# Optimization experiments

Measured on AMD Instinct MI355X. Metric: run time of the kernel, lower is better.

The kernel has to match this reference:

```python
import jax, jax.numpy as jnp
import numpy as np

N_NODES = 50000
N_EDGES = 640000
M_DIM = 128
D_DIM = 128
H_DIM = M_DIM // 2
NORM_EPS = 1e-5


def setup_inputs() -> dict:
    key = jax.random.key(0)
    ks = jax.random.split(key, 8)
    messages = jax.random.normal(ks[0], (N_EDGES, M_DIM), dtype=jnp.float32)
    target_indices = jax.random.randint(ks[1], (N_EDGES,), 0, N_NODES, dtype=jnp.int64)
    node_features = jax.random.normal(ks[2], (N_NODES, D_DIM), dtype=jnp.float32)
    # attention scorer params (torch Linear: weight [out,in])
    W1 = 0.02 * jax.random.normal(ks[3], (H_DIM, M_DIM + D_DIM), dtype=jnp.float32)
    b1 = jnp.zeros((H_DIM,), dtype=jnp.float32)
    W2 = 0.02 * jax.random.normal(ks[4], (1, H_DIM), dtype=jnp.float32)
    gamma = jnp.ones((M_DIM,), dtype=jnp.float32)
    beta = jnp.zeros((M_DIM,), dtype=jnp.float32)
    return {"messages": messages, "target_indices": target_indices,
            "node_features": node_features, "n_nodes": N_NODES,
            "W1": W1, "b1": b1, "W2": W2, "gamma": gamma, "beta": beta}


def reference(messages, target_indices, node_features, n_nodes, W1, b1, W2, gamma, beta):
    # gather target node feats per edge: [E, D]
    target_feats = node_features[target_indices]
    attn_input = jnp.concatenate([messages, target_feats], axis=-1)  # [E, M+D]
    h = jax.nn.gelu(attn_input @ W1.T + b1, approximate=False)       # [E, M//2]
    raw_scores = (h @ W2.T)[:, 0]                                    # [E]
    weights = jax.nn.sigmoid(raw_scores)                             # [E]
    weighted = messages * weights[:, None]                           # [E, M]
    aggregated = jax.ops.segment_sum(weighted, target_indices, num_segments=n_nodes)  # [N, M]
    sum_weights = jax.ops.segment_sum(weights, target_indices, num_segments=n_nodes)  # [N]
    aggregated = aggregated / (sum_weights[:, None] + 1e-8)
    # LayerNorm over last dim
    mu = jnp.mean(aggregated, axis=-1, keepdims=True)
    var = jnp.var(aggregated, axis=-1, keepdims=True)
    normed = (aggregated - mu) * jax.lax.rsqrt(var + NORM_EPS)
    return normed * gamma + beta
```

## Files before the change

kernel.cpp:

```cpp
#include <hip/hip_runtime.h>
#include <hip/hip_bf16.h>

#define EDGES   640000
#define NNODES  50000
#define MDIM    128
#define HDIM    64
#define XSTR    36

typedef __attribute__((ext_vector_type(8))) short bshort8;
typedef __attribute__((ext_vector_type(4))) float f32x4;

__device__ __forceinline__ short f2bf(float f) {
    __hip_bfloat16 h = __float2bfloat16(f);
    return *reinterpret_cast<short*>(&h);
}

__device__ __forceinline__ float gelu_fast(float h) {
    const float x  = h * 0.70710678118654752f;
    const float ax = fabsf(x);
    const float t  = __builtin_amdgcn_rcpf(fmaf(0.3275911f, ax, 1.0f));
    float p = fmaf(1.061405429f, t, -1.453152027f);
    p = fmaf(p, t,  1.421413741f);
    p = fmaf(p, t, -0.284496736f);
    p = fmaf(p, t,  0.254829592f);
    p *= t;
    const float e = __expf(-x * x);
    float er = fmaf(-p, e, 1.0f);
    er = (x < 0.0f) ? -er : er;
    return 0.5f * h * (1.0f + er);
}

__global__ void k0_prep(const float* __restrict__ w1,
                        short* __restrict__ bpack, float* __restrict__ w1dt) {
    const int i = blockIdx.x * 256 + threadIdx.x;
    if (i < 8192) {
        const int ii   = i & 7;
        const int lane = (i >> 3) & 63;
        const int jtkc = i >> 9;
        const int kc = jtkc >> 2, jt = jtkc & 3;
        const int j = jt * 16 + (lane & 15);
        const int k = kc * 32 + (lane >> 4) * 8 + ii;
        bpack[i] = f2bf(w1[j * 256 + k]);
    } else if (i < 16384) {
        const int t = i - 8192;
        const int k = t >> 6, j = t & 63;
        w1dt[t] = w1[j * 256 + 128 + k];
    }
}

__global__ void khist(const int* __restrict__ tgt, int* __restrict__ counts) {
    const int e = blockIdx.x * 256 + threadIdx.x;
    if (e < EDGES) atomicAdd(&counts[tgt[e]], 1);
}

__global__ __launch_bounds__(256, 4) void kg_nodes(
    const float* __restrict__ feats, const float* __restrict__ w1dt,
    const float* __restrict__ b1, float* __restrict__ g)
{
    __shared__ float xs[4][64 * XSTR];
    const int wv = threadIdx.x >> 6, L = threadIdx.x & 63;
    const long base = ((long)blockIdx.x * 4 + wv) * 64;
    float* xb = xs[wv];
    float h[HDIM];
#pragma unroll
    for (int j = 0; j < HDIM; ++j) h[j] = 0.0f;
    const int gq = L >> 3, sub = L & 7;
    for (int c = 0; c < 4; ++c) {
        const int col0 = c * 32;
#pragma unroll
        for (int r = 0; r < 8; ++r) {
            long row = base + gq + 8 * r;
            if (row > NNODES - 1) row = NNODES - 1;
            float4 v = *(const float4*)(feats + row * MDIM + col0 + sub * 4);
            *(float4*)(xb + (gq + 8 * r) * XSTR + sub * 4) = v;
        }
        __syncthreads();
        for (int k4 = 0; k4 < 8; ++k4) {
            const float4 xv = *(const float4*)(xb + L * XSTR + 4 * k4);
            const float* colw = w1dt + (c * 32 + 4 * k4) * HDIM;
            const float xa[4] = {xv.x, xv.y, xv.z, xv.w};
#pragma unroll
            for (int kk = 0; kk < 4; ++kk) {
                const float xk = xa[kk];
#pragma unroll
                for (int j = 0; j < HDIM; ++j)
                    h[j] = fmaf(colw[kk * HDIM + j], xk, h[j]);
            }
        }
        __syncthreads();
    }
    const long row = base + L;
    if (row < NNODES) {
        float* gp = g + row * HDIM;
#pragma unroll
        for (int j4 = 0; j4 < 16; ++j4) {
            float4 b4 = *(const float4*)(b1 + 4 * j4);
            float4 o;
            o.x = h[4 * j4 + 0] + b4.x; o.y = h[4 * j4 + 1] + b4.y;
            o.z = h[4 * j4 + 2] + b4.z; o.w = h[4 * j4 + 3] + b4.w;
            *(float4*)(gp + 4 * j4) = o;
        }
    }
}

__global__ void kscan_local(const int* __restrict__ counts, int* __restrict__ offsets,
                            int* __restrict__ blocksums) {
    __shared__ int s[256];
    const int tid = threadIdx.x;
    const int i = blockIdx.x * 256 + tid;
    int v = (i < NNODES) ? counts[i] : 0;
    s[tid] = v;
    __syncthreads();
    for (int d = 1; d < 256; d <<= 1) {
        int t = (tid >= d) ? s[tid - d] : 0;
        __syncthreads();
        s[tid] += t;
        __syncthreads();
    }
    if (i < NNODES) offsets[i] = s[tid];
    if (tid == 255) blocksums[blockIdx.x] = s[255];
}

__global__ void kscan_blk(int* __restrict__ blocksums, int nblk) {
    __shared__ int s[256];
    const int tid = threadIdx.x;
    int v = (tid < nblk) ? blocksums[tid] : 0;
    s[tid] = v;
    __syncthreads();
    for (int d = 1; d < 256; d <<= 1) {
        int t = (tid >= d) ? s[tid - d] : 0;
        __syncthreads();
        s[tid] += t;
        __syncthreads();
    }
    if (tid < nblk) blocksums[tid] = s[tid] - v;
}

__global__ void kscan_fix(int* __restrict__ offsets, const int* __restrict__ blocksums,
                          const int* __restrict__ counts, int* __restrict__ cursor) {
    const int i = blockIdx.x * 256 + threadIdx.x;
    if (i < NNODES) {
        const int incl = offsets[i] + blocksums[i >> 8];
        offsets[i] = incl;
        cursor[i] = incl - counts[i];
    }
}

__global__ void kscatter(const int* __restrict__ tgt, int* __restrict__ cursor,
                         int* __restrict__ eidx) {
    const int e = blockIdx.x * 256 + threadIdx.x;
    if (e < EDGES) {
        const int pos = atomicAdd(&cursor[tgt[e]], 1);
        eidx[pos] = e;
    }
}

__global__ __launch_bounds__(256, 4) void kfused(
    const float* __restrict__ msgs, const int* __restrict__ eidx,
    const int* __restrict__ offsets, const short* __restrict__ bpack,
    const float* __restrict__ g, const float* __restrict__ w2,
    const float* __restrict__ gamma, const float* __restrict__ beta,
    float* __restrict__ out)
{
    __shared__ float lds[4][16][132];
    const int wv = threadIdx.x >> 6, L = threadIdx.x & 63;
    const int node = blockIdx.x * 4 + wv;
    if (node >= NNODES) return;
    const int end = offsets[node];
    const int beg = (node == 0) ? 0 : offsets[node - 1];
    const int m = end - beg;

    const int n = L & 15, quad = L >> 4;
    float (*xb)[132] = lds[wv];
    const bshort8* bp = (const bshort8*)bpack;

    float w2v[4], gv[4];
    const float* gp = g + (long)node * HDIM;
#pragma unroll
    for (int jt = 0; jt < 4; ++jt) {
        w2v[jt] = w2[jt * 16 + n];
        gv[jt]  = gp[jt * 16 + n];
    }

    float2 acc = {0.0f, 0.0f};
    float swl = 0.0f;

    for (int t0 = 0; t0 < m; t0 += 16) {
        const int sn = t0 + n;
        const int eid = eidx[beg + ((sn < m) ? sn : 0)];
        const float* rp = msgs + (long)eid * MDIM;

        float4 v[8];
#pragma unroll
        for (int kc = 0; kc < 4; ++kc) {
            v[2 * kc]     = *(const float4*)(rp + kc * 32 + quad * 8);
            v[2 * kc + 1] = *(const float4*)(rp + kc * 32 + quad * 8 + 4);
        }
#pragma unroll
        for (int kc = 0; kc < 4; ++kc) {
            *(float4*)(&xb[n][kc * 32 + quad * 8])     = v[2 * kc];
            *(float4*)(&xb[n][kc * 32 + quad * 8 + 4]) = v[2 * kc + 1];
        }

        f32x4 hacc[4];
#pragma unroll
        for (int jt = 0; jt < 4; ++jt) hacc[jt] = (f32x4){0.f, 0.f, 0.f, 0.f};
#pragma unroll
        for (int kc = 0; kc < 4; ++kc) {
            const float4 va = v[2 * kc], vb = v[2 * kc + 1];
            bshort8 a;
            a[0] = f2bf(va.x); a[1] = f2bf(va.y); a[2] = f2bf(va.z); a[3] = f2bf(va.w);
            a[4] = f2bf(vb.x); a[5] = f2bf(vb.y); a[6] = f2bf(vb.z); a[7] = f2bf(vb.w);
#pragma unroll
            for (int jt = 0; jt < 4; ++jt)
                hacc[jt] = __builtin_amdgcn_mfma_f32_16x16x32_bf16(a, bp[(kc * 4 + jt) * 64 + L], hacc[jt], 0, 0, 0);
        }

        float wq[4];
#pragma unroll
        for (int r = 0; r < 4; ++r) {
            float raw = 0.0f;
#pragma unroll
            for (int jt = 0; jt < 4; ++jt) {
                const float hj = hacc[jt][r] + gv[jt];
                raw = fmaf(gelu_fast(hj), w2v[jt], raw);
            }
#pragma unroll
            for (int off = 1; off < 16; off <<= 1)
                raw += __shfl_xor(raw, off, 64);
            const int slot = t0 + quad * 4 + r;
            wq[r] = (slot < m) ? __builtin_amdgcn_rcpf(1.0f + __expf(-raw)) : 0.0f;
        }

#pragma unroll
        for (int i = 0; i < 16; ++i) {
            const float wi = __shfl(wq[i & 3], (i >> 2) << 4, 64);
            swl += wi;
            const float2 mv = *(const float2*)(&xb[i][2 * L]);
            acc.x = fmaf(mv.x, wi, acc.x);
            acc.y = fmaf(mv.y, wi, acc.y);
        }
    }

    float s1 = acc.x + acc.y;
    float s2 = acc.x * acc.x + acc.y * acc.y;
#pragma unroll
    for (int off = 32; off; off >>= 1) {
        s1 += __shfl_xor(s1, off, 64);
        s2 += __shfl_xor(s2, off, 64);
    }
    const float inv = 1.0f / (swl + 1e-8f);
    float2 a;
    a.x = acc.x * inv; a.y = acc.y * inv;
    const float mu = s1 * inv * (1.0f / MDIM);
    const float var = s2 * inv * inv * (1.0f / MDIM) - mu * mu;
    const float rs = rsqrtf(var + 1e-5f);
    const float2 gm = *(const float2*)(gamma + 2 * L);
    const float2 bt = *(const float2*)(beta + 2 * L);
    float2 o;
    o.x = (a.x - mu) * rs * gm.x + bt.x;
    o.y = (a.y - mu) * rs * gm.y + bt.y;
    *(float2*)(out + (long)node * MDIM + 2 * L) = o;
}

extern "C" void kernel_launch(void* const* d_in, const int* in_sizes, int n_in,
                              void* d_out, int out_size, void* d_ws, size_t ws_size,
                              hipStream_t stream) {
    const float* msgs  = (const float*)d_in[0];
    const int*   tgt   = (const int*)d_in[1];
    const float* feats = (const float*)d_in[2];
    const float* W1    = (const float*)d_in[4];
    const float* b1    = (const float*)d_in[5];
    const float* W2    = (const float*)d_in[6];
    const float* gamma = (const float*)d_in[7];
    const float* beta  = (const float*)d_in[8];
    float* out = (float*)d_out;

    char* ws = (char*)d_ws;
    short* bpack   = (short*)(ws + 0);
    float* w1dt    = (float*)(ws + (32 << 10));
    int*   counts  = (int*)  (ws + (64 << 10));
    int*   offsets = (int*)  (ws + (320 << 10));
    int*   cursor  = (int*)  (ws + (576 << 10));
    int*   bsums   = (int*)  (ws + (832 << 10));
    int*   eidx    = (int*)  (ws + (4 << 20));
    float* g       = (float*)(ws + (8 << 20));

    hipMemsetAsync(counts, 0, NNODES * sizeof(int), stream);

    k0_prep<<<64, 256, 0, stream>>>(W1, bpack, w1dt);
    khist<<<(EDGES + 255) / 256, 256, 0, stream>>>(tgt, counts);
    kg_nodes<<<(NNODES + 255) / 256, 256, 0, stream>>>(feats, w1dt, b1, g);
    const int nblk = (NNODES + 255) / 256;
    kscan_local<<<nblk, 256, 0, stream>>>(counts, offsets, bsums);
    kscan_blk<<<1, 256, 0, stream>>>(bsums, nblk);
    kscan_fix<<<nblk, 256, 0, stream>>>(offsets, bsums, counts, cursor);
    kscatter<<<(EDGES + 255) / 256, 256, 0, stream>>>(tgt, cursor, eidx);
    kfused<<<(NNODES + 3) / 4, 256, 0, stream>>>(msgs, eidx, offsets, bpack, g, W2, gamma, beta, out);
}
```

Baseline: 695.7 us.

## Replace LDS staging with register accumulation and butterfly shuffle reduction

Drops the per-wave shared-memory staging of message rows. Each lane now accumulates its own weighted message fragment in 32 registers across the edge loop. After the loop, a transpose-style butterfly of xor shuffles reduces the 16 edge-lanes so that each lane ends up holding two output columns. This removes the LDS writes and the 16 LDS reads per tile, but it raises register pressure (launch bounds of 256,4) and adds a one-time shuffle reduction per node.

```diff
diff --git a/kernel.cpp b/kernel.cpp
--- a/kernel.cpp
+++ b/kernel.cpp
@@ -162,7 +162,6 @@
     const float* __restrict__ gamma, const float* __restrict__ beta,
     float* __restrict__ out)
 {
-    __shared__ float lds[4][16][132];
     const int wv = threadIdx.x >> 6, L = threadIdx.x & 63;
     const int node = blockIdx.x * 4 + wv;
     if (node >= NNODES) return;
@@ -171,7 +170,6 @@
     const int m = end - beg;
 
     const int n = L & 15, quad = L >> 4;
-    float (*xb)[132] = lds[wv];
     const bshort8* bp = (const bshort8*)bpack;
 
     float w2v[4], gv[4];
@@ -182,24 +180,23 @@
         gv[jt]  = gp[jt * 16 + n];
     }
 
-    float2 acc = {0.0f, 0.0f};
+    float4 pacc[8];
+#pragma unroll
+    for (int p = 0; p < 8; ++p) pacc[p] = (float4){0.f, 0.f, 0.f, 0.f};
     float swl = 0.0f;
+
+    const int srcl = (n >> 2) << 4;
 
     for (int t0 = 0; t0 < m; t0 += 16) {
         const int sn = t0 + n;
         const int eid = eidx[beg + ((sn < m) ? sn : 0)];
-        const float* rp = msgs + (long)eid * MDIM;
+        const float* rp = msgs + (long)eid * MDIM + quad * 8;
 
         float4 v[8];
 #pragma unroll
         for (int kc = 0; kc < 4; ++kc) {
-            v[2 * kc]     = *(const float4*)(rp + kc * 32 + quad * 8);
-            v[2 * kc + 1] = *(const float4*)(rp + kc * 32 + quad * 8 + 4);
-        }
-#pragma unroll
-        for (int kc = 0; kc < 4; ++kc) {
-            *(float4*)(&xb[n][kc * 32 + quad * 8])     = v[2 * kc];
-            *(float4*)(&xb[n][kc * 32 + quad * 8 + 4]) = v[2 * kc + 1];
+            v[2 * kc]     = *(const float4*)(rp + kc * 32);
+            v[2 * kc + 1] = *(const float4*)(rp + kc * 32 + 4);
         }
 
         f32x4 hacc[4];
@@ -232,35 +229,91 @@
             wq[r] = (slot < m) ? __builtin_amdgcn_rcpf(1.0f + __expf(-raw)) : 0.0f;
         }
 
-#pragma unroll
-        for (int i = 0; i < 16; ++i) {
-            const float wi = __shfl(wq[i & 3], (i >> 2) << 4, 64);
-            swl += wi;
-            const float2 mv = *(const float2*)(&xb[i][2 * L]);
-            acc.x = fmaf(mv.x, wi, acc.x);
-            acc.y = fmaf(mv.y, wi, acc.y);
-        }
-    }
-
-    float s1 = acc.x + acc.y;
-    float s2 = acc.x * acc.x + acc.y * acc.y;
+        const float ta = __shfl(wq[0], srcl, 64);
+        const float tb = __shfl(wq[1], srcl, 64);
+        const float tc = __shfl(wq[2], srcl, 64);
+        const float td = __shfl(wq[3], srcl, 64);
+        const float t01 = (n & 1) ? tb : ta;
+        const float t23 = (n & 1) ? td : tc;
+        const float wn  = (n & 2) ? t23 : t01;
+        swl += wn;
+
+#pragma unroll
+        for (int p = 0; p < 8; ++p) {
+            pacc[p].x = fmaf(v[p].x, wn, pacc[p].x);
+            pacc[p].y = fmaf(v[p].y, wn, pacc[p].y);
+            pacc[p].z = fmaf(v[p].z, wn, pacc[p].z);
+            pacc[p].w = fmaf(v[p].w, wn, pacc[p].w);
+        }
+    }
+
+    float4 q[4];
+#pragma unroll
+    for (int p = 0; p < 4; ++p) {
+        const float4 keep = (n & 1) ? pacc[p + 4] : pacc[p];
+        const float4 send = (n & 1) ? pacc[p] : pacc[p + 4];
+        float4 rcv;
+        rcv.x = __shfl_xor(send.x, 1, 64);
+        rcv.y = __shfl_xor(send.y, 1, 64);
+        rcv.z = __shfl_xor(send.z, 1, 64);
+        rcv.w = __shfl_xor(send.w, 1, 64);
+        q[p].x = keep.x + rcv.x; q[p].y = keep.y + rcv.y;
+        q[p].z = keep.z + rcv.z; q[p].w = keep.w + rcv.w;
+    }
+    float4 r2[2];
+#pragma unroll
+    for (int p = 0; p < 2; ++p) {
+        const float4 keep = (n & 2) ? q[p + 2] : q[p];
+        const float4 send = (n & 2) ? q[p] : q[p + 2];
+        float4 rcv;
+        rcv.x = __shfl_xor(send.x, 2, 64);
+        rcv.y = __shfl_xor(send.y, 2, 64);
+        rcv.z = __shfl_xor(send.z, 2, 64);
+        rcv.w = __shfl_xor(send.w, 2, 64);
+        r2[p].x = keep.x + rcv.x; r2[p].y = keep.y + rcv.y;
+        r2[p].z = keep.z + rcv.z; r2[p].w = keep.w + rcv.w;
+    }
+    {
+        const float4 keep = (n & 4) ? r2[1] : r2[0];
+        const float4 send = (n & 4) ? r2[0] : r2[1];
+        float4 rcv;
+        rcv.x = __shfl_xor(send.x, 4, 64);
+        rcv.y = __shfl_xor(send.y, 4, 64);
+        rcv.z = __shfl_xor(send.z, 4, 64);
+        rcv.w = __shfl_xor(send.w, 4, 64);
+        r2[0].x = keep.x + rcv.x; r2[0].y = keep.y + rcv.y;
+        r2[0].z = keep.z + rcv.z; r2[0].w = keep.w + rcv.w;
+    }
+    const float kx = (n & 8) ? r2[0].z : r2[0].x;
+    const float ky = (n & 8) ? r2[0].w : r2[0].y;
+    const float sx = (n & 8) ? r2[0].x : r2[0].z;
+    const float sy = (n & 8) ? r2[0].y : r2[0].w;
+    const float S0 = kx + __shfl_xor(sx, 8, 64);
+    const float S1 = ky + __shfl_xor(sy, 8, 64);
+
+    const int co  = (n & 1) * 16 + (n & 2) * 4 + (n & 4) + ((n >> 3) << 1);
+    const int col = (co >> 3) * 32 + quad * 8 + (co & 7);
+
+    float s1 = S0 + S1;
+    float s2 = S0 * S0 + S1 * S1;
+    float sw = swl;
 #pragma unroll
     for (int off = 32; off; off >>= 1) {
         s1 += __shfl_xor(s1, off, 64);
         s2 += __shfl_xor(s2, off, 64);
-    }
-    const float inv = 1.0f / (swl + 1e-8f);
-    float2 a;
-    a.x = acc.x * inv; a.y = acc.y * inv;
+        sw += __shfl_xor(sw, off, 64);
+    }
+    const float inv = 1.0f / (0.25f * sw + 1e-8f);
+    const float a0 = S0 * inv, a1 = S1 * inv;
     const float mu = s1 * inv * (1.0f / MDIM);
     const float var = s2 * inv * inv * (1.0f / MDIM) - mu * mu;
     const float rs = rsqrtf(var + 1e-5f);
-    const float2 gm = *(const float2*)(gamma + 2 * L);
-    const float2 bt = *(const float2*)(beta + 2 * L);
+    const float2 gm = *(const float2*)(gamma + col);
+    const float2 bt = *(const float2*)(beta + col);
     float2 o;
-    o.x = (a.x - mu) * rs * gm.x + bt.x;
-    o.y = (a.y - mu) * rs * gm.y + bt.y;
-    *(float2*)(out + (long)node * MDIM + 2 * L) = o;
+    o.x = (a0 - mu) * rs * gm.x + bt.x;
+    o.y = (a1 - mu) * rs * gm.y + bt.y;
+    *(float2*)(out + (long)node * MDIM + col) = o;
 }
 
 extern "C" void kernel_launch(void* const* d_in, const int* in_sizes, int n_in,
```

Measured after the change: 854.2 us. 1.23x slower.
